# Performance work log

Measured on AMD Instinct MI355X. Metric: run time of the kernel, lower is better.

The kernel has to match this reference:

```python
import jax, jax.numpy as jnp
import numpy as np

# Static config matching init_kwargs / forward constants
H = 12          # num_heads
D = 64          # head_dim
SW = 64         # kv_cache_sliding_window (frames)
SF = 8          # kv_cache_scale_frames
NUM_REG = 4     # num_register_tokens -> camera_idx=0, scale_idx=5
SPECIAL_END = NUM_REG + 2  # camera..scale inclusive slice = tokens [0:6)


def setup_inputs() -> dict:
    key = jax.random.key(0)
    ks = jax.random.split(key, 9)
    B, N, C = 1, 576, 768
    T = 192  # tokens per frame; num_frame_per_block = N // T = 3
    inp = {
        'x': jax.random.normal(ks[0], (B, N, C), jnp.float32),
        'qkv_w': jax.random.normal(ks[1], (3 * C, C), jnp.float32) * (C ** -0.5),
        'qkv_b': jax.random.normal(ks[2], (3 * C,), jnp.float32) * 0.02,
        'proj_w': jax.random.normal(ks[3], (C, C), jnp.float32) * (C ** -0.5),
        'proj_b': jax.random.normal(ks[4], (C,), jnp.float32) * 0.02,
        'k_cache': jax.random.normal(ks[5], (B, H, SW + SF, T, D), jnp.float32),
        'v_cache': jax.random.normal(ks[6], (B, H, SW + SF, T, D), jnp.float32),
        'k_special': jax.random.normal(ks[7], (B, H, 12, SPECIAL_END, D), jnp.float32),
        'v_special': jax.random.normal(ks[8], (B, H, 12, SPECIAL_END, D), jnp.float32),
    }
    return inp


def reference(x, qkv_w, qkv_b, proj_w, proj_b, k_cache, v_cache, k_special, v_special):
    B, N, C = x.shape
    T = k_cache.shape[3]           # tokens per frame
    nfb = N // T                   # num_frame_per_block (inferred, as in torch code)

    # qkv projection: (B,N,3C) -> (3,B,H,N,D)
    qkv = (x @ qkv_w.T + qkv_b).reshape(B, N, 3, H, D).transpose(2, 0, 3, 1, 4)
    q, k, v = qkv[0], qkv[1], qkv[2]   # each (B,H,N,D); q_norm/k_norm = Identity

    # Append new block frames to the cache
    k_cache = jnp.concatenate([k_cache, k.reshape(B, H, nfb, T, D)], axis=2)
    v_cache = jnp.concatenate([v_cache, v.reshape(B, H, nfb, T, D)], axis=2)

    # Sliding-window eviction (shapes chosen so this branch always fires)
    F = k_cache.shape[2]
    evict_start, evict_end = SF, F - SW   # 8 .. 11
    # cross-frame special tokens: camera..scale (tokens 0:6) of evicted frames
    new_sk = k_cache[:, :, evict_start:evict_end, :SPECIAL_END, :]
    new_sv = v_cache[:, :, evict_start:evict_end, :SPECIAL_END, :]
    k_special = jnp.concatenate([k_special, new_sk], axis=2)
    v_special = jnp.concatenate([v_special, new_sv], axis=2)
    # keep scale frames + last sliding_window frames
    k_cache = jnp.concatenate([k_cache[:, :, :SF], k_cache[:, :, -SW:]], axis=2)
    v_cache = jnp.concatenate([v_cache[:, :, :SF], v_cache[:, :, -SW:]], axis=2)

    # Flatten frames -> tokens; prepend special tokens
    k_full = jnp.concatenate([k_special.reshape(B, H, -1, D),
                              k_cache.reshape(B, H, -1, D)], axis=2)
    v_full = jnp.concatenate([v_special.reshape(B, H, -1, D),
                              v_cache.reshape(B, H, -1, D)], axis=2)

    # SDPA (no mask, no dropout, default scale 1/sqrt(D))
    scale = 1.0 / jnp.sqrt(jnp.float32(D))
    scores = jnp.einsum('bhnd,bhmd->bhnm', q, k_full) * scale
    attn = jax.nn.softmax(scores, axis=-1)
    out = jnp.einsum('bhnm,bhmd->bhnd', attn, v_full)

    out = out.transpose(0, 2, 1, 3).reshape(B, N, H * D)
    return out @ proj_w.T + proj_b
```

## Files before the change

### kernel.cpp

```cpp
#include <hip/hip_runtime.h>
#include <hip/hip_bf16.h>

#define NH    12
#define HD    64
#define NT    576
#define CC    768
#define M_TOT 13914
#define MP    13952
#define NTIL  218
#define NEW0  13338

typedef short bf16x8 __attribute__((ext_vector_type(8)));
typedef float f32x4 __attribute__((ext_vector_type(4)));
typedef float f32x16 __attribute__((ext_vector_type(16)));

#define QSCALE 0.18033688011112042f

__device__ __forceinline__ unsigned pk2(float a, float b) {
  __hip_bfloat162 h = __float22bfloat162_rn(make_float2(a, b));
  return *(unsigned*)&h;
}

__device__ __forceinline__ float fexp2(float x) {
  float r;
  asm("v_exp_f32 %0, %1" : "=v"(r) : "v"(x));
  return r;
}

__global__ __launch_bounds__(256) void cvt_all(
    const float* __restrict__ x, const float* __restrict__ wsrc,
    const float* __restrict__ pw, __hip_bfloat16* __restrict__ xb,
    __hip_bfloat16* __restrict__ wb, __hip_bfloat16* __restrict__ wph,
    __hip_bfloat16* __restrict__ wpl) {
  const int nx8 = NT * CC / 8;
  const int nw8 = 3 * CC * CC / 8;
  const int npw8 = CC * CC / 8;
  int i = blockIdx.x * 256 + threadIdx.x;
  if (i < nx8 + nw8) {
    const float* src; __hip_bfloat16* dst; int j;
    if (i < nx8) { src = x; dst = xb; j = i; }
    else { j = i - nx8; src = wsrc; dst = wb; }
    const float4 a = ((const float4*)src)[2 * j];
    const float4 b = ((const float4*)src)[2 * j + 1];
    __hip_bfloat16 t[8];
    t[0] = __float2bfloat16(a.x); t[1] = __float2bfloat16(a.y);
    t[2] = __float2bfloat16(a.z); t[3] = __float2bfloat16(a.w);
    t[4] = __float2bfloat16(b.x); t[5] = __float2bfloat16(b.y);
    t[6] = __float2bfloat16(b.z); t[7] = __float2bfloat16(b.w);
    ((uint4*)dst)[j] = *(const uint4*)t;
  } else {
    const int j = i - nx8 - nw8;
    if (j >= npw8) return;
    float v[8];
    const float4 a = ((const float4*)pw)[2 * j];
    const float4 b = ((const float4*)pw)[2 * j + 1];
    v[0] = a.x; v[1] = a.y; v[2] = a.z; v[3] = a.w;
    v[4] = b.x; v[5] = b.y; v[6] = b.z; v[7] = b.w;
    __hip_bfloat16 th[8], tl[8];
#pragma unroll
    for (int e = 0; e < 8; ++e) {
      th[e] = __float2bfloat16(v[e]);
      tl[e] = __float2bfloat16(v[e] - __bfloat162float(th[e]));
    }
    ((uint4*)wph)[j] = *(const uint4*)th;
    ((uint4*)wpl)[j] = *(const uint4*)tl;
  }
}

__device__ __forceinline__ const float* kv_src_row(
    const float* __restrict__ cache, const float* __restrict__ special,
    int h, int m) {
  if (m < 72) return special + ((size_t)h * 72 + m) * HD;
  if (m < 90) {
    const int j = m - 72;
    return cache + (((size_t)h * 72 + 8 + j / 6) * 192 + (j % 6)) * HD;
  }
  if (m < 1626) return cache + ((size_t)h * 13824 + (m - 90)) * HD;
  return cache + ((size_t)h * 13824 + 2112 + (m - 1626)) * HD;
}

#define GEMM_BLKS 324
#define VT_BLKS   2616
#define KB_BLKS   5002

__global__ __launch_bounds__(256) void qkv_and_gather(
    const __hip_bfloat16* __restrict__ xb, const __hip_bfloat16* __restrict__ wb,
    const float* __restrict__ bias, __hip_bfloat16* __restrict__ Qb,
    __hip_bfloat16* __restrict__ Kf, __hip_bfloat16* __restrict__ Vt,
    const float* __restrict__ kc, const float* __restrict__ ksp,
    const float* __restrict__ vc, const float* __restrict__ vsp) {
  __shared__ float vsf[64][68];
  const int bx = blockIdx.x;
  const int tid = threadIdx.x;

  if (bx < GEMM_BLKS) {
    const int w = tid >> 6, l = tid & 63, l15 = l & 15, lg = l >> 4;
    const int n0 = (bx % 36) * 64;
    const int mw = (bx / 36) * 64 + w * 16;

    f32x4 acc[4];
#pragma unroll
    for (int nt = 0; nt < 4; ++nt) acc[nt] = (f32x4){0.f, 0.f, 0.f, 0.f};

    const __hip_bfloat16* arow = xb + (size_t)(mw + l15) * CC + 8 * lg;
#pragma unroll 4
    for (int k0 = 0; k0 < CC; k0 += 32) {
      const bf16x8 a = *(const bf16x8*)(arow + k0);
#pragma unroll
      for (int nt = 0; nt < 4; ++nt) {
        const bf16x8 b =
            *(const bf16x8*)(wb + (size_t)(n0 + nt * 16 + l15) * CC + k0 + 8 * lg);
        acc[nt] = __builtin_amdgcn_mfma_f32_16x16x32_bf16(a, b, acc[nt], 0, 0, 0);
      }
    }
#pragma unroll
    for (int nt = 0; nt < 4; ++nt) {
      const int c = n0 + nt * 16 + l15;
      const int which = c / CC;
      const int rem = c - which * CC;
      const int hh = rem >> 6;
      const int dd = rem & 63;
      const float bc = bias[c];
#pragma unroll
      for (int r = 0; r < 4; ++r) {
        const int m = mw + 4 * lg + r;
        const float v = acc[nt][r] + bc;
        if (which == 0) {
          Qb[((size_t)hh * NT + m) * HD + dd] = __float2bfloat16(v * QSCALE);
        } else if (which == 1) {
          Kf[((size_t)hh * MP + NEW0 + m) * HD + dd] = __float2bfloat16(v);
        } else {
          Vt[((size_t)hh * HD + dd) * MP + NEW0 + m] = __float2bfloat16(v);
        }
      }
    }
  } else if (bx < GEMM_BLKS + VT_BLKS) {
    const int tv = bx - GEMM_BLKS;
    const int m0 = (tv % 218) * 64;
    const int h = tv / 218;
    if (m0 >= NEW0) return;
#pragma unroll
    for (int p = 0; p < 4; ++p) {
      const int mr = m0 + p * 16 + (tid >> 4);
      const int c4 = (tid & 15) * 4;
      float4 v = make_float4(0.f, 0.f, 0.f, 0.f);
      if (mr < NEW0) v = *(const float4*)(kv_src_row(vc, vsp, h, mr) + c4);
      *(float4*)&vsf[p * 16 + (tid >> 4)][c4] = v;
    }
    __syncthreads();
#pragma unroll
    for (int e0 = 0; e0 < 2; ++e0) {
      const int e = tid + e0 * 256;
      const int d = e >> 3;
      const int ms = (e & 7) * 8;
      __hip_bfloat16 t[8];
#pragma unroll
      for (int j = 0; j < 8; ++j) t[j] = __float2bfloat16(vsf[ms + j][d]);
      __hip_bfloat16* dst = Vt + ((size_t)h * HD + d) * MP + m0 + ms;
      if (m0 + ms + 8 <= NEW0) {
        *(uint4*)dst = *(const uint4*)t;
      } else {
#pragma unroll
        for (int j = 0; j < 8; ++j)
          if (m0 + ms + j < NEW0) dst[j] = t[j];
      }
    }
  } else {
    const int idx = (bx - GEMM_BLKS - VT_BLKS) * 256 + tid;
    const int per_h = NEW0 * 8;
    if (idx >= NH * per_h) return;
    const int h = idx / per_h;
    const int r = idx - h * per_h;
    const int m = r >> 3;
    const int d8 = (r & 7) << 3;
    const float* src = kv_src_row(kc, ksp, h, m) + d8;
    const float4 v0 = *(const float4*)src;
    const float4 v1 = *(const float4*)(src + 4);
    uint4 o;
    o.x = pk2(v0.x, v0.y);
    o.y = pk2(v0.z, v0.w);
    o.z = pk2(v1.x, v1.y);
    o.w = pk2(v1.z, v1.w);
    *(uint4*)(Kf + ((size_t)h * MP + m) * HD + d8) = o;
  }
}

template <int S>
__global__ __launch_bounds__(256, 4) void attn_partial(
    const __hip_bfloat16* __restrict__ Qb, const __hip_bfloat16* __restrict__ Kf,
    const __hip_bfloat16* __restrict__ Vt, float* __restrict__ Opart,
    float2* __restrict__ mlpart) {
  __shared__ __align__(16) char lds[16384];
  char* ksb = lds;
  char* vtb = lds + 8192;

  const int tid = threadIdx.x;
  const int w = tid >> 6, l = tid & 63;
  const int l31 = l & 31, hi = l >> 5;

  const int i = blockIdx.x;
  const int per_xcd = (5 * NH * S) / 8;
  const int work = (i & 7) * per_xcd + (i >> 3);
  const int qt = work % 5;
  const int hs = work / 5;
  const int h = hs % NH;
  const int strip = hs / NH;

  const int qrow = qt * 128 + w * 32 + l31;
  const int qrc = qrow < NT ? qrow : NT - 1;

  bf16x8 qreg[4];
  {
    const __hip_bfloat16* qp = Qb + ((size_t)h * NT + qrc) * HD + 8 * hi;
#pragma unroll
    for (int s4 = 0; s4 < 4; ++s4) qreg[s4] = *(const bf16x8*)(qp + 16 * s4);
  }

  f32x16 oacc0, oacc1;
#pragma unroll
  for (int r = 0; r < 16; ++r) { oacc0[r] = 0.f; oacc1[r] = 0.f; }
  float m_run = -1e30f, l_run = 0.f;

  const __hip_bfloat16* Kh = Kf + (size_t)h * MP * HD;
  const __hip_bfloat16* Vth = Vt + (size_t)h * HD * MP;

  for (int t = strip; t < NTIL; t += S) {
    const int m0 = t * 64;
#pragma unroll
    for (int e = 0; e < 2; ++e) {
      const int c = tid + 256 * e;
      const int row = c >> 3, p = c & 7;
      const unsigned off = ((unsigned)((row << 7) | (p << 4))) ^ ((row & 7) << 4);
      const uint4 kd = *(const uint4*)(Kh + (size_t)(m0 + row) * HD + p * 8);
      const uint4 vd = *(const uint4*)(Vth + (size_t)row * MP + m0 + p * 8);
      *(uint4*)(ksb + off) = kd;
      *(uint4*)(vtb + off) = vd;
    }
    __syncthreads();

    f32x16 sc0, sc1;
#pragma unroll
    for (int r = 0; r < 16; ++r) { sc0[r] = 0.f; sc1[r] = 0.f; }
#pragma unroll
    for (int s4 = 0; s4 < 4; ++s4) {
      const int cb = 32 * s4 + 16 * hi;
      const unsigned o0 = ((unsigned)((l31 << 7) | cb)) ^ ((l31 & 7) << 4);
      const unsigned o1 = ((unsigned)(((l31 + 32) << 7) | cb)) ^ ((l31 & 7) << 4);
      const bf16x8 a0 = *(const bf16x8*)(ksb + o0);
      const bf16x8 a1 = *(const bf16x8*)(ksb + o1);
      sc0 = __builtin_amdgcn_mfma_f32_32x32x16_bf16(a0, qreg[s4], sc0, 0, 0, 0);
      sc1 = __builtin_amdgcn_mfma_f32_32x32x16_bf16(a1, qreg[s4], sc1, 0, 0, 0);
    }

    if (m0 + 64 > M_TOT) {
#pragma unroll
      for (int r = 0; r < 16; ++r) {
        const int base = (r & 3) + 8 * (r >> 2) + 4 * hi;
        if (m0 + base >= M_TOT) sc0[r] = -1e30f;
        if (m0 + 32 + base >= M_TOT) sc1[r] = -1e30f;
      }
    }

    float t8[8];
#pragma unroll
    for (int r2 = 0; r2 < 8; ++r2)
      t8[r2] = fmaxf(fmaxf(sc0[r2], sc0[r2 + 8]), fmaxf(sc1[r2], sc1[r2 + 8]));
#pragma unroll
    for (int r2 = 0; r2 < 4; ++r2) t8[r2] = fmaxf(t8[r2], t8[r2 + 4]);
    float mt = fmaxf(fmaxf(t8[0], t8[1]), fmaxf(t8[2], t8[3]));
    mt = fmaxf(mt, __shfl_xor(mt, 32));

    if (__any(mt > m_run + 8.f)) {
      const float mn = fmaxf(m_run, mt);
      const float corr = fexp2(m_run - mn);
      m_run = mn;
      l_run *= corr;
#pragma unroll
      for (int r = 0; r < 16; ++r) { oacc0[r] *= corr; oacc1[r] *= corr; }
    }

    unsigned W0[8], W1[8];
    float s8[8];
#pragma unroll
    for (int i2 = 0; i2 < 8; ++i2) {
      const float e0 = fexp2(sc0[2 * i2] - m_run);
      const float e1 = fexp2(sc0[2 * i2 + 1] - m_run);
      const float f0 = fexp2(sc1[2 * i2] - m_run);
      const float f1 = fexp2(sc1[2 * i2 + 1] - m_run);
      W0[i2] = pk2(e0, e1);
      W1[i2] = pk2(f0, f1);
      s8[i2] = (e0 + e1) + (f0 + f1);
    }
#pragma unroll
    for (int i2 = 0; i2 < 4; ++i2) s8[i2] += s8[i2 + 4];
    float psum = (s8[0] + s8[1]) + (s8[2] + s8[3]);
    psum += __shfl_xor(psum, 32);
    l_run += psum;

#pragma unroll
    for (int s4 = 0; s4 < 4; ++s4) {
      const int u = s4 & 1;
      const unsigned a0 = (s4 < 2) ? W0[4 * u + 0] : W1[4 * u + 0];
      const unsigned a1 = (s4 < 2) ? W0[4 * u + 1] : W1[4 * u + 1];
      const unsigned a2 = (s4 < 2) ? W0[4 * u + 2] : W1[4 * u + 2];
      const unsigned a3 = (s4 < 2) ? W0[4 * u + 3] : W1[4 * u + 3];
      const unsigned x0 = (unsigned)__shfl_xor((int)a0, 32);
      const unsigned x1 = (unsigned)__shfl_xor((int)a1, 32);
      const unsigned x2 = (unsigned)__shfl_xor((int)a2, 32);
      const unsigned x3 = (unsigned)__shfl_xor((int)a3, 32);
      union { unsigned u4[4]; bf16x8 v; } pa;
      pa.u4[0] = hi ? x2 : a0;
      pa.u4[1] = hi ? x3 : a1;
      pa.u4[2] = hi ? a2 : x0;
      pa.u4[3] = hi ? a3 : x1;
      const int cb = 32 * s4 + 16 * hi;
#pragma unroll
      for (int dh = 0; dh < 2; ++dh) {
        const int vr = 32 * dh + l31;
        const unsigned ov = ((unsigned)((vr << 7) | cb)) ^ ((vr & 7) << 4);
        const bf16x8 va = *(const bf16x8*)(vtb + ov);
        if (dh == 0)
          oacc0 = __builtin_amdgcn_mfma_f32_32x32x16_bf16(va, pa.v, oacc0, 0, 0, 0);
        else
          oacc1 = __builtin_amdgcn_mfma_f32_32x32x16_bf16(va, pa.v, oacc1, 0, 0, 0);
      }
    }
    __syncthreads();
  }

  if (qrow < NT) {
    float* Op = Opart + (((size_t)strip * NH + h) * NT + qrow) * HD;
#pragma unroll
    for (int g = 0; g < 4; ++g) {
      f32x4 o0 = {oacc0[4 * g], oacc0[4 * g + 1], oacc0[4 * g + 2], oacc0[4 * g + 3]};
      f32x4 o1 = {oacc1[4 * g], oacc1[4 * g + 1], oacc1[4 * g + 2], oacc1[4 * g + 3]};
      *(f32x4*)(Op + 8 * g + 4 * hi) = o0;
      *(f32x4*)(Op + 32 + 8 * g + 4 * hi) = o1;
    }
    if (hi == 0)
      mlpart[((size_t)strip * NH + h) * NT + qrow] = make_float2(m_run, l_run);
  }
}

template <int S>
__global__ __launch_bounds__(256) void attn_merge(
    const float* __restrict__ Opart, const float2* __restrict__ mlpart,
    __hip_bfloat16* __restrict__ Owh, __hip_bfloat16* __restrict__ Owl) {
  const int idx = blockIdx.x * 256 + threadIdx.x;
  if (idx >= NH * NT * HD) return;
  const int d = idx & 63;
  const int hn = idx >> 6;
  const int n = hn % NT;
  const int h = hn / NT;
  float M = -1e30f;
  float m[S], lv[S];
#pragma unroll
  for (int s = 0; s < S; ++s) {
    const float2 ml = mlpart[((size_t)s * NH + h) * NT + n];
    m[s] = ml.x; lv[s] = ml.y;
    M = fmaxf(M, m[s]);
  }
  float L = 0.f, O = 0.f;
#pragma unroll
  for (int s = 0; s < S; ++s) {
    const float e = fexp2(m[s] - M);
    L += lv[s] * e;
    O += Opart[(((size_t)s * NH + h) * NT + n) * HD + d] * e;
  }
  const float v = O / L;
  const __hip_bfloat16 hB = __float2bfloat16(v);
  const size_t o = (size_t)n * CC + h * HD + d;
  Owh[o] = hB;
  Owl[o] = __float2bfloat16(v - __bfloat162float(hB));
}

__global__ __launch_bounds__(256) void gemm_proj_mfma(
    const __hip_bfloat16* __restrict__ Ah, const __hip_bfloat16* __restrict__ Al,
    const __hip_bfloat16* __restrict__ Wh, const __hip_bfloat16* __restrict__ Wl,
    const float* __restrict__ bias, float* __restrict__ out_f) {
  const int tid = threadIdx.x;
  const int w = tid >> 6, l = tid & 63, l15 = l & 15, lg = l >> 4;
  const int n0 = blockIdx.x * 32 + (w >> 1) * 16;
  const int mw = blockIdx.y * 32 + (w & 1) * 16;

  f32x4 acc = (f32x4){0.f, 0.f, 0.f, 0.f};

  const __hip_bfloat16* ah = Ah + (size_t)(mw + l15) * CC + 8 * lg;
  const __hip_bfloat16* al = Al + (size_t)(mw + l15) * CC + 8 * lg;
#pragma unroll 4
  for (int k0 = 0; k0 < CC; k0 += 32) {
    const bf16x8 a0 = *(const bf16x8*)(ah + k0);
    const bf16x8 a1 = *(const bf16x8*)(al + k0);
    const size_t wi = (size_t)(n0 + l15) * CC + k0 + 8 * lg;
    const bf16x8 bh = *(const bf16x8*)(Wh + wi);
    const bf16x8 bl = *(const bf16x8*)(Wl + wi);
    acc = __builtin_amdgcn_mfma_f32_16x16x32_bf16(a0, bh, acc, 0, 0, 0);
    acc = __builtin_amdgcn_mfma_f32_16x16x32_bf16(a0, bl, acc, 0, 0, 0);
    acc = __builtin_amdgcn_mfma_f32_16x16x32_bf16(a1, bh, acc, 0, 0, 0);
  }
  const int c = n0 + l15;
  const float bc = bias[c];
#pragma unroll
  for (int r = 0; r < 4; ++r)
    out_f[(size_t)(mw + 4 * lg + r) * CC + c] = acc[r] + bc;
}

extern "C" void kernel_launch(void* const* d_in, const int* in_sizes, int n_in,
                              void* d_out, int out_size, void* d_ws,
                              size_t ws_size, hipStream_t stream) {
  const float* x       = (const float*)d_in[0];
  const float* qkv_w   = (const float*)d_in[1];
  const float* qkv_b   = (const float*)d_in[2];
  const float* proj_w  = (const float*)d_in[3];
  const float* proj_b  = (const float*)d_in[4];
  const float* k_cache = (const float*)d_in[5];
  const float* v_cache = (const float*)d_in[6];
  const float* k_specl = (const float*)d_in[7];
  const float* v_specl = (const float*)d_in[8];
  float* out = (float*)d_out;

  const size_t qb_bytes = (size_t)NH * NT * HD * 2;
  const size_t kv_bytes = (size_t)NH * MP * HD * 2;
  const size_t xb_bytes = (size_t)NT * CC * 2;
  const size_t wb_bytes = (size_t)3 * CC * CC * 2;
  const size_t pw_bytes = (size_t)CC * CC * 2;
  const size_t owh_bytes = (size_t)NT * CC * 2;

  auto need = [&](int S) -> size_t {
    const size_t op = (size_t)S * NH * NT * HD * 4;
    const size_t ml = (size_t)S * NH * NT * 8;
    const size_t opr = op > xb_bytes + wb_bytes ? op : xb_bytes + wb_bytes;
    return qb_bytes + 2 * kv_bytes + opr + ml + 2 * pw_bytes;
  };
  const int S = (need(16) <= ws_size) ? 16 : 8;
  const size_t op_bytes = (size_t)S * NH * NT * HD * 4;
  const size_t ml_bytes = (size_t)S * NH * NT * 8;
  const size_t opr = op_bytes > xb_bytes + wb_bytes ? op_bytes : xb_bytes + wb_bytes;

  char* ws = (char*)d_ws;
  __hip_bfloat16* Qb = (__hip_bfloat16*)ws;
  char* kf_region = ws + qb_bytes;
  __hip_bfloat16* Kf = (__hip_bfloat16*)kf_region;
  __hip_bfloat16* Vt = (__hip_bfloat16*)(kf_region + kv_bytes);
  char* opp = kf_region + 2 * kv_bytes;
  float* Opart = (float*)opp;
  __hip_bfloat16* xb = (__hip_bfloat16*)opp;
  __hip_bfloat16* wb = (__hip_bfloat16*)(opp + xb_bytes);
  float2* mlpart = (float2*)(opp + opr);
  __hip_bfloat16* wph = (__hip_bfloat16*)(opp + opr + ml_bytes);
  __hip_bfloat16* wpl = (__hip_bfloat16*)(opp + opr + ml_bytes + pw_bytes);
  __hip_bfloat16* Owh = (__hip_bfloat16*)kf_region;
  __hip_bfloat16* Owl = (__hip_bfloat16*)(kf_region + owh_bytes);

  cvt_all<<<dim3(1368), 256, 0, stream>>>(x, qkv_w, proj_w, xb, wb, wph, wpl);
  qkv_and_gather<<<dim3(GEMM_BLKS + VT_BLKS + KB_BLKS), 256, 0, stream>>>(
      xb, wb, qkv_b, Qb, Kf, Vt, k_cache, k_specl, v_cache, v_specl);
  if (S == 16) {
    attn_partial<16><<<dim3(5 * NH * 16), 256, 0, stream>>>(Qb, Kf, Vt, Opart, mlpart);
    attn_merge<16><<<dim3((NH * NT * HD + 255) / 256), 256, 0, stream>>>(
        Opart, mlpart, Owh, Owl);
  } else {
    attn_partial<8><<<dim3(5 * NH * 8), 256, 0, stream>>>(Qb, Kf, Vt, Opart, mlpart);
    attn_merge<8><<<dim3((NH * NT * HD + 255) / 256), 256, 0, stream>>>(
        Opart, mlpart, Owh, Owl);
  }
  gemm_proj_mfma<<<dim3(24, 18), 256, 0, stream>>>(Owh, Owl, wph, wpl, proj_b, out);
}
```

Measured before the change: 122.7 us.

## Double-buffer K/V tiles via direct global-to-LDS DMA loads in attention

Replaces the register-staged K/V tile loads with global_load_lds DMA into a double-buffered 32KB LDS region. The next tile is prefetched while the current one is computed, with vmcnt waits and raw barriers in place of __syncthreads. The goal is to hide global load latency and drop the VGPR round trip. The cost is doubled LDS per block, which may limit occupancy at 4 blocks per CU, and hand-managed wait counts that are fragile.

```diff
diff --git a/kernel.cpp b/kernel.cpp
--- a/kernel.cpp
+++ b/kernel.cpp
@@ -25,6 +25,12 @@
   float r;
   asm("v_exp_f32 %0, %1" : "=v"(r) : "v"(x));
   return r;
+}
+
+__device__ __forceinline__ void dma16(const void* g, void* l) {
+  __builtin_amdgcn_global_load_lds(
+      (const __attribute__((address_space(1))) unsigned int*)g,
+      (__attribute__((address_space(3))) unsigned int*)l, 16, 0, 0);
 }
 
 __global__ __launch_bounds__(256) void cvt_all(
@@ -190,9 +196,7 @@
     const __hip_bfloat16* __restrict__ Qb, const __hip_bfloat16* __restrict__ Kf,
     const __hip_bfloat16* __restrict__ Vt, float* __restrict__ Opart,
     float2* __restrict__ mlpart) {
-  __shared__ __align__(16) char lds[16384];
-  char* ksb = lds;
-  char* vtb = lds + 8192;
+  __shared__ __align__(16) char lds[32768];
 
   const int tid = threadIdx.x;
   const int w = tid >> 6, l = tid & 63;
@@ -224,19 +228,45 @@
   const __hip_bfloat16* Kh = Kf + (size_t)h * MP * HD;
   const __hip_bfloat16* Vth = Vt + (size_t)h * HD * MP;
 
+  const int row0 = w * 8 + (l >> 3);
+  const int row1 = 32 + row0;
+  const int p0 = (l & 7) ^ (row0 & 7);
+  const int p1 = (l & 7) ^ (row1 & 7);
+  const size_t kOff0 = (size_t)row0 * HD + p0 * 8;
+  const size_t kOff1 = (size_t)row1 * HD + p1 * 8;
+  const size_t vOff0 = (size_t)row0 * MP + p0 * 8;
+  const size_t vOff1 = (size_t)row1 * MP + p1 * 8;
+  const int ldsA = w * 1024;
+  const int ldsB = (4 + w) * 1024;
+
+  auto issue = [&](int t, char* buf) {
+    const size_t mK = (size_t)t * 64 * HD;
+    const int mV = t * 64;
+    dma16(Kh + mK + kOff0, buf + ldsA);
+    dma16(Kh + mK + kOff1, buf + ldsB);
+    dma16(Vth + vOff0 + mV, buf + 8192 + ldsA);
+    dma16(Vth + vOff1 + mV, buf + 8192 + ldsB);
+  };
+
+  asm volatile("s_waitcnt vmcnt(0)" ::: "memory");
+  issue(strip, lds);
+
+  int cur = 0;
   for (int t = strip; t < NTIL; t += S) {
+    const int tn = t + S;
+    char* ksb = lds + (cur << 14);
+    char* vtb = ksb + 8192;
+
+    if (tn < NTIL) {
+      issue(tn, lds + ((cur ^ 1) << 14));
+      asm volatile("s_waitcnt vmcnt(4)" ::: "memory");
+    } else {
+      asm volatile("s_waitcnt vmcnt(0)" ::: "memory");
+    }
+    __builtin_amdgcn_s_barrier();
+    __builtin_amdgcn_sched_barrier(0);
+
     const int m0 = t * 64;
-#pragma unroll
-    for (int e = 0; e < 2; ++e) {
-      const int c = tid + 256 * e;
-      const int row = c >> 3, p = c & 7;
-      const unsigned off = ((unsigned)((row << 7) | (p << 4))) ^ ((row & 7) << 4);
-      const uint4 kd = *(const uint4*)(Kh + (size_t)(m0 + row) * HD + p * 8);
-      const uint4 vd = *(const uint4*)(Vth + (size_t)row * MP + m0 + p * 8);
-      *(uint4*)(ksb + off) = kd;
-      *(uint4*)(vtb + off) = vd;
-    }
-    __syncthreads();
 
     f32x16 sc0, sc1;
 #pragma unroll
@@ -325,7 +355,10 @@
           oacc1 = __builtin_amdgcn_mfma_f32_32x32x16_bf16(va, pa.v, oacc1, 0, 0, 0);
       }
     }
-    __syncthreads();
+
+    __builtin_amdgcn_sched_barrier(0);
+    __builtin_amdgcn_s_barrier();
+    cur ^= 1;
   }
 
   if (qrow < NT) {
```

Result: slower. 127.5 us (+3.9%).

## Stage 128-key tiles per barrier and raise wave priority around MFMA blocks

Applied to the files above, without the earlier changes.

The attention kernel now loads 128 keys of K and V^T into a doubled 32KB LDS buffer per iteration and processes them as two 64-key sub-tiles, halving the number of barriers and loop iterations. It also wraps the MFMA sections in s_setprio to favour waves issuing matrix ops. The larger LDS footprint may reduce occupancy at 4 blocks per CU. With 109 tiles, strips also get coarser, which can worsen load balance.

```diff
diff --git a/kernel.cpp b/kernel.cpp
--- a/kernel.cpp
+++ b/kernel.cpp
@@ -7,7 +7,7 @@
 #define CC    768
 #define M_TOT 13914
 #define MP    13952
-#define NTIL  218
+#define NT128 109
 #define NEW0  13338
 
 typedef short bf16x8 __attribute__((ext_vector_type(8)));
@@ -190,9 +190,7 @@
     const __hip_bfloat16* __restrict__ Qb, const __hip_bfloat16* __restrict__ Kf,
     const __hip_bfloat16* __restrict__ Vt, float* __restrict__ Opart,
     float2* __restrict__ mlpart) {
-  __shared__ __align__(16) char lds[16384];
-  char* ksb = lds;
-  char* vtb = lds + 8192;
+  __shared__ __align__(16) char lds[32768];
 
   const int tid = threadIdx.x;
   const int w = tid >> 6, l = tid & 63;
@@ -224,105 +222,125 @@
   const __hip_bfloat16* Kh = Kf + (size_t)h * MP * HD;
   const __hip_bfloat16* Vth = Vt + (size_t)h * HD * MP;
 
-  for (int t = strip; t < NTIL; t += S) {
-    const int m0 = t * 64;
-#pragma unroll
-    for (int e = 0; e < 2; ++e) {
+  for (int t = strip; t < NT128; t += S) {
+    const int m0 = t * 128;
+#pragma unroll
+    for (int e = 0; e < 4; ++e) {
       const int c = tid + 256 * e;
       const int row = c >> 3, p = c & 7;
-      const unsigned off = ((unsigned)((row << 7) | (p << 4))) ^ ((row & 7) << 4);
-      const uint4 kd = *(const uint4*)(Kh + (size_t)(m0 + row) * HD + p * 8);
-      const uint4 vd = *(const uint4*)(Vth + (size_t)row * MP + m0 + p * 8);
-      *(uint4*)(ksb + off) = kd;
-      *(uint4*)(vtb + off) = vd;
+      const int u = row >> 6, ri = row & 63;
+      const unsigned off =
+          (unsigned)(u * 8192) + (((unsigned)((ri << 7) | (p << 4))) ^ ((ri & 7) << 4));
+      *(uint4*)(lds + off) = *(const uint4*)(Kh + (size_t)(m0 + row) * HD + p * 8);
+    }
+#pragma unroll
+    for (int e = 0; e < 4; ++e) {
+      const int c = tid + 256 * e;
+      const int u = c >> 9, rem = c & 511;
+      const int d = rem >> 3, p = rem & 7;
+      const unsigned off = 16384u +
+          (unsigned)(u * 8192) + (((unsigned)((d << 7) | (p << 4))) ^ ((d & 7) << 4));
+      *(uint4*)(lds + off) =
+          *(const uint4*)(Vth + (size_t)d * MP + m0 + u * 64 + p * 8);
     }
     __syncthreads();
 
-    f32x16 sc0, sc1;
-#pragma unroll
-    for (int r = 0; r < 16; ++r) { sc0[r] = 0.f; sc1[r] = 0.f; }
-#pragma unroll
-    for (int s4 = 0; s4 < 4; ++s4) {
-      const int cb = 32 * s4 + 16 * hi;
-      const unsigned o0 = ((unsigned)((l31 << 7) | cb)) ^ ((l31 & 7) << 4);
-      const unsigned o1 = ((unsigned)(((l31 + 32) << 7) | cb)) ^ ((l31 & 7) << 4);
-      const bf16x8 a0 = *(const bf16x8*)(ksb + o0);
-      const bf16x8 a1 = *(const bf16x8*)(ksb + o1);
-      sc0 = __builtin_amdgcn_mfma_f32_32x32x16_bf16(a0, qreg[s4], sc0, 0, 0, 0);
-      sc1 = __builtin_amdgcn_mfma_f32_32x32x16_bf16(a1, qreg[s4], sc1, 0, 0, 0);
-    }
-
-    if (m0 + 64 > M_TOT) {
-#pragma unroll
-      for (int r = 0; r < 16; ++r) {
-        const int base = (r & 3) + 8 * (r >> 2) + 4 * hi;
-        if (m0 + base >= M_TOT) sc0[r] = -1e30f;
-        if (m0 + 32 + base >= M_TOT) sc1[r] = -1e30f;
-      }
-    }
-
-    float t8[8];
-#pragma unroll
-    for (int r2 = 0; r2 < 8; ++r2)
-      t8[r2] = fmaxf(fmaxf(sc0[r2], sc0[r2 + 8]), fmaxf(sc1[r2], sc1[r2 + 8]));
-#pragma unroll
-    for (int r2 = 0; r2 < 4; ++r2) t8[r2] = fmaxf(t8[r2], t8[r2 + 4]);
-    float mt = fmaxf(fmaxf(t8[0], t8[1]), fmaxf(t8[2], t8[3]));
-    mt = fmaxf(mt, __shfl_xor(mt, 32));
-
-    if (__any(mt > m_run + 8.f)) {
-      const float mn = fmaxf(m_run, mt);
-      const float corr = fexp2(m_run - mn);
-      m_run = mn;
-      l_run *= corr;
-#pragma unroll
-      for (int r = 0; r < 16; ++r) { oacc0[r] *= corr; oacc1[r] *= corr; }
-    }
-
-    unsigned W0[8], W1[8];
-    float s8[8];
-#pragma unroll
-    for (int i2 = 0; i2 < 8; ++i2) {
-      const float e0 = fexp2(sc0[2 * i2] - m_run);
-      const float e1 = fexp2(sc0[2 * i2 + 1] - m_run);
-      const float f0 = fexp2(sc1[2 * i2] - m_run);
-      const float f1 = fexp2(sc1[2 * i2 + 1] - m_run);
-      W0[i2] = pk2(e0, e1);
-      W1[i2] = pk2(f0, f1);
-      s8[i2] = (e0 + e1) + (f0 + f1);
-    }
-#pragma unroll
-    for (int i2 = 0; i2 < 4; ++i2) s8[i2] += s8[i2 + 4];
-    float psum = (s8[0] + s8[1]) + (s8[2] + s8[3]);
-    psum += __shfl_xor(psum, 32);
-    l_run += psum;
-
-#pragma unroll
-    for (int s4 = 0; s4 < 4; ++s4) {
-      const int u = s4 & 1;
-      const unsigned a0 = (s4 < 2) ? W0[4 * u + 0] : W1[4 * u + 0];
-      const unsigned a1 = (s4 < 2) ? W0[4 * u + 1] : W1[4 * u + 1];
-      const unsigned a2 = (s4 < 2) ? W0[4 * u + 2] : W1[4 * u + 2];
-      const unsigned a3 = (s4 < 2) ? W0[4 * u + 3] : W1[4 * u + 3];
-      const unsigned x0 = (unsigned)__shfl_xor((int)a0, 32);
-      const unsigned x1 = (unsigned)__shfl_xor((int)a1, 32);
-      const unsigned x2 = (unsigned)__shfl_xor((int)a2, 32);
-      const unsigned x3 = (unsigned)__shfl_xor((int)a3, 32);
-      union { unsigned u4[4]; bf16x8 v; } pa;
-      pa.u4[0] = hi ? x2 : a0;
-      pa.u4[1] = hi ? x3 : a1;
-      pa.u4[2] = hi ? a2 : x0;
-      pa.u4[3] = hi ? a3 : x1;
-      const int cb = 32 * s4 + 16 * hi;
-#pragma unroll
-      for (int dh = 0; dh < 2; ++dh) {
-        const int vr = 32 * dh + l31;
-        const unsigned ov = ((unsigned)((vr << 7) | cb)) ^ ((vr & 7) << 4);
-        const bf16x8 va = *(const bf16x8*)(vtb + ov);
-        if (dh == 0)
-          oacc0 = __builtin_amdgcn_mfma_f32_32x32x16_bf16(va, pa.v, oacc0, 0, 0, 0);
-        else
-          oacc1 = __builtin_amdgcn_mfma_f32_32x32x16_bf16(va, pa.v, oacc1, 0, 0, 0);
+#pragma unroll
+    for (int u = 0; u < 2; ++u) {
+      char* ksb = lds + u * 8192;
+      char* vtb = lds + 16384 + u * 8192;
+      const int mu = m0 + u * 64;
+
+      f32x16 sc0, sc1;
+#pragma unroll
+      for (int r = 0; r < 16; ++r) { sc0[r] = 0.f; sc1[r] = 0.f; }
+      __builtin_amdgcn_s_setprio(1);
+#pragma unroll
+      for (int s4 = 0; s4 < 4; ++s4) {
+        const int cb = 32 * s4 + 16 * hi;
+        const unsigned o0 = ((unsigned)((l31 << 7) | cb)) ^ ((l31 & 7) << 4);
+        const unsigned o1 = ((unsigned)(((l31 + 32) << 7) | cb)) ^ ((l31 & 7) << 4);
+        const bf16x8 a0 = *(const bf16x8*)(ksb + o0);
+        const bf16x8 a1 = *(const bf16x8*)(ksb + o1);
+        sc0 = __builtin_amdgcn_mfma_f32_32x32x16_bf16(a0, qreg[s4], sc0, 0, 0, 0);
+        sc1 = __builtin_amdgcn_mfma_f32_32x32x16_bf16(a1, qreg[s4], sc1, 0, 0, 0);
+      }
+      __builtin_amdgcn_s_setprio(0);
+
+      if (mu + 64 > M_TOT) {
+#pragma unroll
+        for (int r = 0; r < 16; ++r) {
+          const int base = (r & 3) + 8 * (r >> 2) + 4 * hi;
+          if (mu + base >= M_TOT) sc0[r] = -1e30f;
+          if (mu + 32 + base >= M_TOT) sc1[r] = -1e30f;
+        }
+      }
+
+      float t8[8];
+#pragma unroll
+      for (int r2 = 0; r2 < 8; ++r2)
+        t8[r2] = fmaxf(fmaxf(sc0[r2], sc0[r2 + 8]), fmaxf(sc1[r2], sc1[r2 + 8]));
+#pragma unroll
+      for (int r2 = 0; r2 < 4; ++r2) t8[r2] = fmaxf(t8[r2], t8[r2 + 4]);
+      float mt = fmaxf(fmaxf(t8[0], t8[1]), fmaxf(t8[2], t8[3]));
+      mt = fmaxf(mt, __shfl_xor(mt, 32));
+
+      if (__any(mt > m_run + 8.f)) {
+        const float mn = fmaxf(m_run, mt);
+        const float corr = fexp2(m_run - mn);
+        m_run = mn;
+        l_run *= corr;
+#pragma unroll
+        for (int r = 0; r < 16; ++r) { oacc0[r] *= corr; oacc1[r] *= corr; }
+      }
+
+      unsigned W0[8], W1[8];
+      float s8[8];
+#pragma unroll
+      for (int i2 = 0; i2 < 8; ++i2) {
+        const float e0 = fexp2(sc0[2 * i2] - m_run);
+        const float e1 = fexp2(sc0[2 * i2 + 1] - m_run);
+        const float f0 = fexp2(sc1[2 * i2] - m_run);
+        const float f1 = fexp2(sc1[2 * i2 + 1] - m_run);
+        W0[i2] = pk2(e0, e1);
+        W1[i2] = pk2(f0, f1);
+        s8[i2] = (e0 + e1) + (f0 + f1);
+      }
+#pragma unroll
+      for (int i2 = 0; i2 < 4; ++i2) s8[i2] += s8[i2 + 4];
+      float psum = (s8[0] + s8[1]) + (s8[2] + s8[3]);
+      psum += __shfl_xor(psum, 32);
+      l_run += psum;
+
+#pragma unroll
+      for (int s4 = 0; s4 < 4; ++s4) {
+        const int uu = s4 & 1;
+        const unsigned a0 = (s4 < 2) ? W0[4 * uu + 0] : W1[4 * uu + 0];
+        const unsigned a1 = (s4 < 2) ? W0[4 * uu + 1] : W1[4 * uu + 1];
+        const unsigned a2 = (s4 < 2) ? W0[4 * uu + 2] : W1[4 * uu + 2];
+        const unsigned a3 = (s4 < 2) ? W0[4 * uu + 3] : W1[4 * uu + 3];
+        const unsigned x0 = (unsigned)__shfl_xor((int)a0, 32);
+        const unsigned x1 = (unsigned)__shfl_xor((int)a1, 32);
+        const unsigned x2 = (unsigned)__shfl_xor((int)a2, 32);
+        const unsigned x3 = (unsigned)__shfl_xor((int)a3, 32);
+        union { unsigned u4[4]; bf16x8 v; } pa;
+        pa.u4[0] = hi ? x2 : a0;
+        pa.u4[1] = hi ? x3 : a1;
+        pa.u4[2] = hi ? a2 : x0;
+        pa.u4[3] = hi ? a3 : x1;
+        const int cb = 32 * s4 + 16 * hi;
+        __builtin_amdgcn_s_setprio(1);
+#pragma unroll
+        for (int dh = 0; dh < 2; ++dh) {
+          const int vr = 32 * dh + l31;
+          const unsigned ov = ((unsigned)((vr << 7) | cb)) ^ ((vr & 7) << 4);
+          const bf16x8 va = *(const bf16x8*)(vtb + ov);
+          if (dh == 0)
+            oacc0 = __builtin_amdgcn_mfma_f32_32x32x16_bf16(va, pa.v, oacc0, 0, 0, 0);
+          else
+            oacc1 = __builtin_amdgcn_mfma_f32_32x32x16_bf16(va, pa.v, oacc1, 0, 0, 0);
+        }
+        __builtin_amdgcn_s_setprio(0);
       }
     }
     __syncthreads();
```

Result: slower. 130.2 us (+6.1%).
